# Optimization experiments

Hardware: AMD Instinct MI355X
Metric: run time of the kernel (lower is better)

The kernel has to match this reference:

```python
import jax, jax.numpy as jnp
import numpy as np

D_MODEL = 16   # output feature dim of channel_proj
D_STATE = 8
D_CONV = 2
D_INNER = 4    # expand * inner mamba d_model (2*2)
DT_RANK = 1    # ceil(2/16)
NUM_PAIRS = 36
B, W, T = 8, 8, 1024


def setup_inputs() -> dict:
    key = jax.random.key(0)
    ks = jax.random.split(key, 12)
    s = 0.5
    return {
        "raw_signals": jax.random.normal(ks[0], (B, W, NUM_PAIRS, 2, T), jnp.float32),
        "in_proj_w": jax.random.normal(ks[1], (2 * D_INNER, 2), jnp.float32) * s,
        "conv_w": jax.random.normal(ks[2], (D_INNER, D_CONV), jnp.float32) * s,
        "conv_b": jax.random.normal(ks[3], (D_INNER,), jnp.float32) * 0.1,
        "x_proj_w": jax.random.normal(ks[4], (DT_RANK + 2 * D_STATE, D_INNER), jnp.float32) * s,
        "dt_proj_w": jax.random.normal(ks[5], (D_INNER, DT_RANK), jnp.float32) * s,
        "dt_proj_b": jax.random.normal(ks[6], (D_INNER,), jnp.float32) * 0.1,
        # S4D-real init: A_log = log(arange(1..d_state)) per inner channel
        "A_log": jnp.log(jnp.broadcast_to(jnp.arange(1, D_STATE + 1, dtype=jnp.float32), (D_INNER, D_STATE))),
        "D_skip": jnp.ones((D_INNER,), jnp.float32),
        "out_proj_w": jax.random.normal(ks[7], (2, D_INNER), jnp.float32) * s,
        "proj_w": jax.random.normal(ks[8], (D_MODEL, 2), jnp.float32) * s,
        "proj_b": jax.random.normal(ks[9], (D_MODEL,), jnp.float32) * 0.1,
    }


def _mamba_forward(x_in, in_proj_w, conv_w, conv_b, x_proj_w, dt_proj_w,
                   dt_proj_b, A_log, D_skip, out_proj_w):
    # x_in: (N, T, 2)
    N, Tlen, _ = x_in.shape
    xz = jnp.einsum('ntc,dc->ntd', x_in, in_proj_w)          # (N,T,2*d_inner)
    x, z = jnp.split(xz, 2, axis=-1)                          # (N,T,d_inner) each
    # causal depthwise conv1d, kernel size D_CONV
    xp = jnp.pad(x, ((0, 0), (D_CONV - 1, 0), (0, 0)))
    x = sum(xp[:, k:k + Tlen] * conv_w[:, k] for k in range(D_CONV)) + conv_b
    x = jax.nn.silu(x)
    # input-dependent dt, B, C
    x_dbl = jnp.einsum('ntd,ed->nte', x, x_proj_w)            # (N,T,dt_rank+2*d_state)
    dt, Bm, Cm = jnp.split(x_dbl, [DT_RANK, DT_RANK + D_STATE], axis=-1)
    dt = jax.nn.softplus(jnp.einsum('ntr,dr->ntd', dt, dt_proj_w) + dt_proj_b)
    A = -jnp.exp(A_log)                                       # (d_inner,d_state)
    deltaA = jnp.exp(dt[..., None] * A)                       # (N,T,d_inner,d_state)
    deltaBx = dt[..., None] * Bm[:, :, None, :] * x[..., None]

    def step(h, inputs):
        dA_t, dBx_t, c_t = inputs
        h = dA_t * h + dBx_t                                  # (N,d_inner,d_state)
        y_t = jnp.einsum('nds,ns->nd', h, c_t)
        return h, y_t

    h0 = jnp.zeros((N, D_INNER, D_STATE), x.dtype)
    _, ys = jax.lax.scan(
        step, h0,
        (deltaA.transpose(1, 0, 2, 3), deltaBx.transpose(1, 0, 2, 3), Cm.transpose(1, 0, 2)))
    y = ys.transpose(1, 0, 2) + x * D_skip                    # (N,T,d_inner)
    y = y * jax.nn.silu(z)
    return jnp.einsum('ntd,cd->ntc', y, out_proj_w)           # (N,T,2)


def reference(raw_signals, in_proj_w, conv_w, conv_b, x_proj_w, dt_proj_w,
              dt_proj_b, A_log, D_skip, out_proj_w, proj_w, proj_b):
    Bsz, Wn, P, C, Tlen = raw_signals.shape
    # per-window loop in torch does identical math -> flatten windows into batch
    x_in = raw_signals.transpose(0, 1, 2, 4, 3).reshape(-1, Tlen, C)  # (B*W*P, T, 2)
    out = _mamba_forward(x_in, in_proj_w, conv_w, conv_b, x_proj_w, dt_proj_w,
                         dt_proj_b, A_log, D_skip, out_proj_w)
    feat = out.mean(axis=1)                                   # (B*W*P, 2)
    proj = jax.nn.relu(feat @ proj_w.T + proj_b)              # dropout is eval no-op
    proj = proj.reshape(Bsz, Wn, P, -1)                       # (B,W,P,d_model)
    return proj.mean(axis=2)                                  # (B,W,d_model)
```

## Files before the change

kernel.cpp:

```cpp
#include <hip/hip_runtime.h>


#define TT 1024
#define TC 32
#define GSEG 4
#define SEGLEN (TT / GSEG)
#define NCHUNK (SEGLEN / TC)
#define NUM_PAIRS 36
#define NSEQ 2304
#define ST 36
#define PER_HALF (TC * ST)
#define HALF_SHIFT 16
#define PER_WAVE (2 * PER_HALF + HALF_SHIFT)
#define STAGE_TOTAL (GSEG * PER_WAVE)
#define COMB_OFF STAGE_TOTAL
#define COMB_SZ (2 * GSEG * 32 * 2)
#define PART_OFF (COMB_OFF + COMB_SZ)
#define PART_SZ (2 * GSEG * 2)
#define LDS_TOTAL (PART_OFF + PART_SZ)

__device__ __forceinline__ float fast_sigmoid(float v) {
    return __builtin_amdgcn_rcpf(1.0f + __expf(-v));
}

__global__ __launch_bounds__(256, 4)
void pm_kernel(const float* __restrict__ raw,
               const float* __restrict__ in_proj_w,
               const float* __restrict__ conv_w,
               const float* __restrict__ conv_b,
               const float* __restrict__ x_proj_w,
               const float* __restrict__ dt_proj_w,
               const float* __restrict__ dt_proj_b,
               const float* __restrict__ A_log,
               const float* __restrict__ D_skip,
               const float* __restrict__ out_proj_w,
               const float* __restrict__ proj_w,
               const float* __restrict__ proj_b,
               float* __restrict__ out)
{
    __shared__ float lds[LDS_TOTAL];

    const int tid  = threadIdx.x;
    const int wid  = tid >> 6;
    const int lane = tid & 63;
    const int half = lane >> 5;
    const int lh   = lane & 31;
    const int n    = blockIdx.x * 2 + half;
    const float* rp = raw + (size_t)n * (2 * TT);

    float* stg = lds + wid * PER_WAVE + half * (PER_HALF + HALF_SHIFT);

    float ipw[8][2];
#pragma unroll
    for (int j = 0; j < 8; ++j) { ipw[j][0] = in_proj_w[2*j]; ipw[j][1] = in_proj_w[2*j+1]; }
    float cw0[4], cw1[4], cbv[4], dpw[4], dpb[4], Dsk[4], ow0[4], ow1[4];
#pragma unroll
    for (int d = 0; d < 4; ++d) {
        cw0[d] = conv_w[2*d]; cw1[d] = conv_w[2*d+1]; cbv[d] = conv_b[d];
        dpw[d] = dt_proj_w[d]; dpb[d] = dt_proj_b[d];
        Dsk[d] = D_skip[d]; ow0[d] = out_proj_w[d]; ow1[d] = out_proj_w[4+d];
    }
    float xpw[17][4];
#pragma unroll
    for (int e = 0; e < 17; ++e)
#pragma unroll
        for (int d = 0; d < 4; ++d) xpw[e][d] = x_proj_w[4*e + d];

    const float LOG2E = 1.4426950408889634f;
    const int   d_idx = lh >> 3;
    const int   s_idx = lh & 7;
    const float A2ds  = -__expf(A_log[lh]) * LOG2E;
    const float owd0  = out_proj_w[d_idx];
    const float owd1  = out_proj_w[4 + d_idx];

    float A_run = 1.0f, hB = 0.0f, W = 0.0f, S = 0.0f;
    float sacc0 = 0.f, sacc1 = 0.f;

    const int seg0 = wid * SEGLEN;

    int t0 = seg0 + lh;
    float c0  = rp[t0];
    float c1  = rp[TT + t0];
    float c0m = (t0 > 0) ? rp[t0 - 1]      : 0.0f;
    float c1m = (t0 > 0) ? rp[TT + t0 - 1] : 0.0f;

    for (int chunk = 0; chunk < NCHUNK; ++chunk) {
        float p0 = 0.f, p1 = 0.f, p0m = 0.f, p1m = 0.f;
        if (chunk + 1 < NCHUNK) {
            int tn = seg0 + (chunk + 1) * TC + lh;
            p0  = rp[tn];       p1  = rp[TT + tn];
            p0m = rp[tn - 1];   p1m = rp[TT + tn - 1];
        }

        float xz[8], xm1[4];
#pragma unroll
        for (int j = 0; j < 8; ++j) xz[j] = ipw[j][0]*c0 + ipw[j][1]*c1;
#pragma unroll
        for (int d = 0; d < 4; ++d) xm1[d] = ipw[d][0]*c0m + ipw[d][1]*c1m;

        float x[4], sz[4];
#pragma unroll
        for (int d = 0; d < 4; ++d) {
            float v = xm1[d]*cw0[d] + xz[d]*cw1[d] + cbv[d];
            x[d] = v * fast_sigmoid(v);
            float zv = xz[4 + d];
            sz[d] = zv * fast_sigmoid(zv);
        }

        float dtin = xpw[0][0]*x[0] + xpw[0][1]*x[1] + xpw[0][2]*x[2] + xpw[0][3]*x[3];
        float Bm[8], Cm[8];
#pragma unroll
        for (int s = 0; s < 8; ++s) {
            Bm[s] = xpw[1+s][0]*x[0] + xpw[1+s][1]*x[1] + xpw[1+s][2]*x[2] + xpw[1+s][3]*x[3];
            Cm[s] = xpw[9+s][0]*x[0] + xpw[9+s][1]*x[1] + xpw[9+s][2]*x[2] + xpw[9+s][3]*x[3];
        }

        float* slot = stg + lh * ST;
#pragma unroll
        for (int d = 0; d < 4; ++d) {
            float v = dtin*dpw[d] + dpb[d];
            float dt = fmaxf(v, 0.0f) + __logf(1.0f + __expf(-fabsf(v)));
            *(float4*)(slot + 4*d) = make_float4(dt, dt * x[d], sz[d], 0.0f);
            float g = x[d] * Dsk[d] * sz[d];
            sacc0 = fmaf(g, ow0[d], sacc0);
            sacc1 = fmaf(g, ow1[d], sacc1);
        }
#pragma unroll
        for (int s = 0; s < 8; ++s)
            *(float2*)(slot + 16 + 2*s) = make_float2(Bm[s], Cm[s]);

        __asm__ volatile("s_waitcnt lgkmcnt(0)" ::: "memory");

#pragma unroll
        for (int t2 = 0; t2 < TC; ++t2) {
            const float* sl = stg + t2 * ST;
            float4 dv = *(const float4*)(sl + 4*d_idx);
            float2 bc = *(const float2*)(sl + 16 + 2*s_idx);
            float a = exp2f(dv.x * A2ds);
            float b = dv.y * bc.x;
            float q = bc.y * dv.z;
            A_run *= a;
            hB = fmaf(a, hB, b);
            W  = fmaf(A_run, q, W);
            S  = fmaf(hB, q, S);
        }

        __asm__ volatile("s_waitcnt lgkmcnt(0)" ::: "memory");

        c0 = p0; c1 = p1; c0m = p0m; c1m = p1m;
    }

    float* comb = lds + COMB_OFF;
    *(float2*)(comb + ((half*GSEG + wid)*32 + lh)*2) = make_float2(A_run, hB);
    __syncthreads();

    float h_in = 0.0f;
#pragma unroll
    for (int g = 0; g < GSEG; ++g) {
        if (g < wid) {
            float2 abg = *(const float2*)(comb + ((half*GSEG + g)*32 + lh)*2);
            h_in = fmaf(abg.x, h_in, abg.y);
        }
    }

    float F = fmaf(h_in, W, S);
    float tot0 = fmaf(F, owd0, sacc0);
    float tot1 = fmaf(F, owd1, sacc1);
#pragma unroll
    for (int m = 16; m >= 1; m >>= 1) {
        tot0 += __shfl_xor(tot0, m, 64);
        tot1 += __shfl_xor(tot1, m, 64);
    }
    float* part = lds + PART_OFF;
    if (lh == 0) {
        part[(half*GSEG + wid)*2]     = tot0;
        part[(half*GSEG + wid)*2 + 1] = tot1;
    }
    __syncthreads();

    if (wid == 0 && lh < 16) {
        float f0 = 0.f, f1 = 0.f;
#pragma unroll
        for (int g = 0; g < GSEG; ++g) {
            f0 += part[(half*GSEG + g)*2];
            f1 += part[(half*GSEG + g)*2 + 1];
        }
        f0 *= (1.0f / (float)TT);
        f1 *= (1.0f / (float)TT);
        float pv = f0*proj_w[2*lh] + f1*proj_w[2*lh + 1] + proj_b[lh];
        pv = fmaxf(pv, 0.0f);
        atomicAdd(out + (n / NUM_PAIRS) * 16 + lh, pv * (1.0f / NUM_PAIRS));
    }
}

extern "C" void kernel_launch(void* const* d_in, const int* in_sizes, int n_in,
                              void* d_out, int out_size, void* d_ws, size_t ws_size,
                              hipStream_t stream)
{
    const float* raw        = (const float*)d_in[0];
    const float* in_proj_w  = (const float*)d_in[1];
    const float* conv_w     = (const float*)d_in[2];
    const float* conv_b     = (const float*)d_in[3];
    const float* x_proj_w   = (const float*)d_in[4];
    const float* dt_proj_w  = (const float*)d_in[5];
    const float* dt_proj_b  = (const float*)d_in[6];
    const float* A_log      = (const float*)d_in[7];
    const float* D_skip     = (const float*)d_in[8];
    const float* out_proj_w = (const float*)d_in[9];
    const float* proj_w     = (const float*)d_in[10];
    const float* proj_b     = (const float*)d_in[11];

    hipMemsetAsync(d_out, 0, (size_t)out_size * sizeof(float), stream);

    pm_kernel<<<dim3(NSEQ / 2), dim3(256), 0, stream>>>(
        raw, in_proj_w, conv_w, conv_b, x_proj_w, dt_proj_w, dt_proj_b,
        A_log, D_skip, out_proj_w, proj_w, proj_b, (float*)d_out);
}
```

Baseline: 145.0 us.

## Double time segments per block, pack B/C in fp16, use packed v2f FMA math

Doubles the number of time segments per sequence from 4 to 8, so each block now runs 512 threads and each wave handles a shorter segment. The B/C staging in LDS moves from fp32 to half precision, shrinking slot size. Most arithmetic is recast as two-wide vector FMAs so the compiler can emit packed fp32 instructions, and the A_run/hB/W/S recurrences are merged into vector form. The combine and partial-sum buffers reuse the staging LDS after an extra barrier. The trade-offs are fp16 rounding of B and C, a longer cross-segment combine, and higher register and LDS pressure per block.

```diff
diff --git a/kernel.cpp b/kernel.cpp
--- a/kernel.cpp
+++ b/kernel.cpp
@@ -1,29 +1,29 @@
 #include <hip/hip_runtime.h>
-
+#include <hip/hip_fp16.h>
+
+
+typedef float v2f __attribute__((ext_vector_type(2)));
 
 #define TT 1024
 #define TC 32
-#define GSEG 4
+#define GSEG 8
 #define SEGLEN (TT / GSEG)
 #define NCHUNK (SEGLEN / TC)
 #define NUM_PAIRS 36
 #define NSEQ 2304
-#define ST 36
-#define PER_HALF (TC * ST)
+
+#define SLOTF 24
+#define PER_HALF (TC * SLOTF)
 #define HALF_SHIFT 16
 #define PER_WAVE (2 * PER_HALF + HALF_SHIFT)
 #define STAGE_TOTAL (GSEG * PER_WAVE)
-#define COMB_OFF STAGE_TOTAL
-#define COMB_SZ (2 * GSEG * 32 * 2)
-#define PART_OFF (COMB_OFF + COMB_SZ)
-#define PART_SZ (2 * GSEG * 2)
-#define LDS_TOTAL (PART_OFF + PART_SZ)
-
-__device__ __forceinline__ float fast_sigmoid(float v) {
-    return __builtin_amdgcn_rcpf(1.0f + __expf(-v));
+
+__device__ __forceinline__ float fast_silu(float v) {
+    float e = __builtin_amdgcn_exp2f(v * -1.4426950408889634f);
+    return v * __builtin_amdgcn_rcpf(1.0f + e);
 }
 
-__global__ __launch_bounds__(256, 4)
+__global__ __launch_bounds__(512, 6)
 void pm_kernel(const float* __restrict__ raw,
                const float* __restrict__ in_proj_w,
                const float* __restrict__ conv_w,
@@ -38,7 +38,7 @@
                const float* __restrict__ proj_b,
                float* __restrict__ out)
 {
-    __shared__ float lds[LDS_TOTAL];
+    __shared__ float lds[STAGE_TOTAL];
 
     const int tid  = threadIdx.x;
     const int wid  = tid >> 6;
@@ -50,31 +50,44 @@
 
     float* stg = lds + wid * PER_WAVE + half * (PER_HALF + HALF_SHIFT);
 
-    float ipw[8][2];
-#pragma unroll
-    for (int j = 0; j < 8; ++j) { ipw[j][0] = in_proj_w[2*j]; ipw[j][1] = in_proj_w[2*j+1]; }
-    float cw0[4], cw1[4], cbv[4], dpw[4], dpb[4], Dsk[4], ow0[4], ow1[4];
+    v2f ipc0[4], ipc1[4];
+#pragma unroll
+    for (int k = 0; k < 4; ++k) {
+        ipc0[k] = (v2f){in_proj_w[4*k],     in_proj_w[4*k + 2]};
+        ipc1[k] = (v2f){in_proj_w[4*k + 1], in_proj_w[4*k + 3]};
+    }
+    v2f cw0p[2], cw1p[2], cbp[2];
+#pragma unroll
+    for (int k = 0; k < 2; ++k) {
+        cw0p[k] = (v2f){conv_w[4*k],     conv_w[4*k + 2]};
+        cw1p[k] = (v2f){conv_w[4*k + 1], conv_w[4*k + 3]};
+        cbp[k]  = (v2f){conv_b[2*k],     conv_b[2*k + 1]};
+    }
+    float dpw[4], dpb[4], xp0[4];
+    v2f owp[4];
+    float Dsk[4];
 #pragma unroll
     for (int d = 0; d < 4; ++d) {
-        cw0[d] = conv_w[2*d]; cw1[d] = conv_w[2*d+1]; cbv[d] = conv_b[d];
         dpw[d] = dt_proj_w[d]; dpb[d] = dt_proj_b[d];
-        Dsk[d] = D_skip[d]; ow0[d] = out_proj_w[d]; ow1[d] = out_proj_w[4+d];
-    }
-    float xpw[17][4];
-#pragma unroll
-    for (int e = 0; e < 17; ++e)
-#pragma unroll
-        for (int d = 0; d < 4; ++d) xpw[e][d] = x_proj_w[4*e + d];
+        xp0[d] = x_proj_w[d];  Dsk[d] = D_skip[d];
+        owp[d] = (v2f){out_proj_w[d], out_proj_w[4 + d]};
+    }
+    v2f xbc[8][4];
+#pragma unroll
+    for (int s = 0; s < 8; ++s)
+#pragma unroll
+        for (int d = 0; d < 4; ++d)
+            xbc[s][d] = (v2f){x_proj_w[4*(1+s) + d], x_proj_w[4*(9+s) + d]};
 
     const float LOG2E = 1.4426950408889634f;
     const int   d_idx = lh >> 3;
     const int   s_idx = lh & 7;
     const float A2ds  = -__expf(A_log[lh]) * LOG2E;
-    const float owd0  = out_proj_w[d_idx];
-    const float owd1  = out_proj_w[4 + d_idx];
-
-    float A_run = 1.0f, hB = 0.0f, W = 0.0f, S = 0.0f;
-    float sacc0 = 0.f, sacc1 = 0.f;
+    const v2f   owd   = (v2f){out_proj_w[d_idx], out_proj_w[4 + d_idx]};
+
+    v2f AhB = {1.0f, 0.0f};
+    v2f WS  = {0.0f, 0.0f};
+    v2f sacc = {0.0f, 0.0f};
 
     const int seg0 = wid * SEGLEN;
 
@@ -92,57 +105,74 @@
             p0m = rp[tn - 1];   p1m = rp[TT + tn - 1];
         }
 
-        float xz[8], xm1[4];
-#pragma unroll
-        for (int j = 0; j < 8; ++j) xz[j] = ipw[j][0]*c0 + ipw[j][1]*c1;
-#pragma unroll
-        for (int d = 0; d < 4; ++d) xm1[d] = ipw[d][0]*c0m + ipw[d][1]*c1m;
+        const v2f c0v = {c0, c0}, c1v = {c1, c1}, c0mv = {c0m, c0m}, c1mv = {c1m, c1m};
+        v2f xzp[4], xm1p[2];
+#pragma unroll
+        for (int k = 0; k < 4; ++k)
+            xzp[k] = __builtin_elementwise_fma(ipc0[k], c0v, ipc1[k] * c1v);
+#pragma unroll
+        for (int k = 0; k < 2; ++k)
+            xm1p[k] = __builtin_elementwise_fma(ipc0[k], c0mv, ipc1[k] * c1mv);
 
         float x[4], sz[4];
 #pragma unroll
+        for (int k = 0; k < 2; ++k) {
+            v2f v = __builtin_elementwise_fma(xm1p[k], cw0p[k],
+                    __builtin_elementwise_fma(xzp[k], cw1p[k], cbp[k]));
+            x[2*k]   = fast_silu(v.x);
+            x[2*k+1] = fast_silu(v.y);
+            sz[2*k]   = fast_silu(xzp[2 + k].x);
+            sz[2*k+1] = fast_silu(xzp[2 + k].y);
+        }
+
+        float dtin = xp0[0]*x[0] + xp0[1]*x[1] + xp0[2]*x[2] + xp0[3]*x[3];
+        v2f bc[8];
+#pragma unroll
+        for (int s = 0; s < 8; ++s) {
+            v2f a = xbc[s][0] * (v2f){x[0], x[0]};
+            a = __builtin_elementwise_fma(xbc[s][1], (v2f){x[1], x[1]}, a);
+            a = __builtin_elementwise_fma(xbc[s][2], (v2f){x[2], x[2]}, a);
+            bc[s] = __builtin_elementwise_fma(xbc[s][3], (v2f){x[3], x[3]}, a);
+        }
+
+        float* slot = stg + lh * SLOTF;
+#pragma unroll
         for (int d = 0; d < 4; ++d) {
-            float v = xm1[d]*cw0[d] + xz[d]*cw1[d] + cbv[d];
-            x[d] = v * fast_sigmoid(v);
-            float zv = xz[4 + d];
-            sz[d] = zv * fast_sigmoid(zv);
-        }
-
-        float dtin = xpw[0][0]*x[0] + xpw[0][1]*x[1] + xpw[0][2]*x[2] + xpw[0][3]*x[3];
-        float Bm[8], Cm[8];
-#pragma unroll
-        for (int s = 0; s < 8; ++s) {
-            Bm[s] = xpw[1+s][0]*x[0] + xpw[1+s][1]*x[1] + xpw[1+s][2]*x[2] + xpw[1+s][3]*x[3];
-            Cm[s] = xpw[9+s][0]*x[0] + xpw[9+s][1]*x[1] + xpw[9+s][2]*x[2] + xpw[9+s][3]*x[3];
-        }
-
-        float* slot = stg + lh * ST;
-#pragma unroll
-        for (int d = 0; d < 4; ++d) {
-            float v = dtin*dpw[d] + dpb[d];
-            float dt = fmaxf(v, 0.0f) + __logf(1.0f + __expf(-fabsf(v)));
+            float u = dtin*dpw[d] + dpb[d];
+            float dt = fmaxf(u, 0.0f) + __logf(1.0f + __expf(-fabsf(u)));
             *(float4*)(slot + 4*d) = make_float4(dt, dt * x[d], sz[d], 0.0f);
             float g = x[d] * Dsk[d] * sz[d];
-            sacc0 = fmaf(g, ow0[d], sacc0);
-            sacc1 = fmaf(g, ow1[d], sacc1);
-        }
-#pragma unroll
-        for (int s = 0; s < 8; ++s)
-            *(float2*)(slot + 16 + 2*s) = make_float2(Bm[s], Cm[s]);
+            sacc = __builtin_elementwise_fma((v2f){g, g}, owp[d], sacc);
+        }
+        uint4 ubc0, ubc1;
+        {
+            __half2 h0 = __floats2half2_rn(bc[0].x, bc[0].y);
+            __half2 h1 = __floats2half2_rn(bc[1].x, bc[1].y);
+            __half2 h2 = __floats2half2_rn(bc[2].x, bc[2].y);
+            __half2 h3 = __floats2half2_rn(bc[3].x, bc[3].y);
+            __half2 h4 = __floats2half2_rn(bc[4].x, bc[4].y);
+            __half2 h5 = __floats2half2_rn(bc[5].x, bc[5].y);
+            __half2 h6 = __floats2half2_rn(bc[6].x, bc[6].y);
+            __half2 h7 = __floats2half2_rn(bc[7].x, bc[7].y);
+            ubc0 = make_uint4(*(uint*)&h0, *(uint*)&h1, *(uint*)&h2, *(uint*)&h3);
+            ubc1 = make_uint4(*(uint*)&h4, *(uint*)&h5, *(uint*)&h6, *(uint*)&h7);
+        }
+        *(uint4*)(slot + 16) = ubc0;
+        *(uint4*)(slot + 20) = ubc1;
 
         __asm__ volatile("s_waitcnt lgkmcnt(0)" ::: "memory");
 
 #pragma unroll
         for (int t2 = 0; t2 < TC; ++t2) {
-            const float* sl = stg + t2 * ST;
-            float4 dv = *(const float4*)(sl + 4*d_idx);
-            float2 bc = *(const float2*)(sl + 16 + 2*s_idx);
-            float a = exp2f(dv.x * A2ds);
-            float b = dv.y * bc.x;
-            float q = bc.y * dv.z;
-            A_run *= a;
-            hB = fmaf(a, hB, b);
-            W  = fmaf(A_run, q, W);
-            S  = fmaf(hB, q, S);
+            const float* sl = stg + t2 * SLOTF;
+            float4 f = *(const float4*)(sl + 4*d_idx);
+            uint ub  = *(const uint*)(sl + 16 + s_idx);
+            float2 bcf = __half22float2(*(__half2*)&ub);
+            float a = __builtin_amdgcn_exp2f(f.x * A2ds);
+            float b = f.y * bcf.x;
+            float q = f.z * bcf.y;
+            AhB = __builtin_elementwise_fma((v2f){a, a}, AhB, (v2f){0.0f, b});
+            WS  = __builtin_elementwise_fma(AhB, (v2f){q, q}, WS);
         }
 
         __asm__ volatile("s_waitcnt lgkmcnt(0)" ::: "memory");
@@ -150,28 +180,29 @@
         c0 = p0; c1 = p1; c0m = p0m; c1m = p1m;
     }
 
-    float* comb = lds + COMB_OFF;
-    *(float2*)(comb + ((half*GSEG + wid)*32 + lh)*2) = make_float2(A_run, hB);
+    __syncthreads();
+    float2* comb = (float2*)lds;
+    comb[(half*GSEG + wid)*32 + lh] = make_float2(AhB.x, AhB.y);
     __syncthreads();
 
     float h_in = 0.0f;
 #pragma unroll
     for (int g = 0; g < GSEG; ++g) {
         if (g < wid) {
-            float2 abg = *(const float2*)(comb + ((half*GSEG + g)*32 + lh)*2);
+            float2 abg = comb[(half*GSEG + g)*32 + lh];
             h_in = fmaf(abg.x, h_in, abg.y);
         }
     }
 
-    float F = fmaf(h_in, W, S);
-    float tot0 = fmaf(F, owd0, sacc0);
-    float tot1 = fmaf(F, owd1, sacc1);
+    float F = fmaf(h_in, WS.x, WS.y);
+    v2f tot = __builtin_elementwise_fma((v2f){F, F}, owd, sacc);
+    float tot0 = tot.x, tot1 = tot.y;
 #pragma unroll
     for (int m = 16; m >= 1; m >>= 1) {
         tot0 += __shfl_xor(tot0, m, 64);
         tot1 += __shfl_xor(tot1, m, 64);
     }
-    float* part = lds + PART_OFF;
+    float* part = lds + 2048;
     if (lh == 0) {
         part[(half*GSEG + wid)*2]     = tot0;
         part[(half*GSEG + wid)*2 + 1] = tot1;
@@ -212,7 +243,7 @@
 
     hipMemsetAsync(d_out, 0, (size_t)out_size * sizeof(float), stream);
 
-    pm_kernel<<<dim3(NSEQ / 2), dim3(256), 0, stream>>>(
+    pm_kernel<<<dim3(NSEQ / 2), dim3(512), 0, stream>>>(
         raw, in_proj_w, conv_w, conv_b, x_proj_w, dt_proj_w, dt_proj_b,
         A_log, D_skip, out_proj_w, proj_w, proj_b, (float*)d_out);
 }
```

Result: faster. 133.4 us (-8.0%).

## Pack scan operands to fp16, double time segments, restructure LDS staging

Applied to the files above, without the earlier changes.

Splits each sequence into 8 time segments across 8 waves instead of 4, launching 512-thread blocks. Packs dt*x, silu(z), B and C into fp16 pairs and uses a packed half multiply in the inner scan loop. Replaces the LDS staging layout with separate dt, ds and BC arrays, the BC array padded with an odd stride. Also swaps in raw exp2/log/rcp intrinsics for silu and softplus and vectorises the B/C projection with float2 FMAs. The fp16 rounding of scan inputs lowers precision. The new softplus form can overflow for large inputs.

```diff
diff --git a/kernel.cpp b/kernel.cpp
--- a/kernel.cpp
+++ b/kernel.cpp
@@ -1,29 +1,38 @@
 #include <hip/hip_runtime.h>
-
+#include <hip/hip_fp16.h>
+
+
+typedef float v2f __attribute__((ext_vector_type(2)));
 
 #define TT 1024
 #define TC 32
-#define GSEG 4
+#define GSEG 8
 #define SEGLEN (TT / GSEG)
 #define NCHUNK (SEGLEN / TC)
 #define NUM_PAIRS 36
 #define NSEQ 2304
-#define ST 36
-#define PER_HALF (TC * ST)
-#define HALF_SHIFT 16
-#define PER_WAVE (2 * PER_HALF + HALF_SHIFT)
+
+#define DT_OFF 0
+#define DS_OFF 128
+#define BC_OFF 256
+#define BC_STRIDE 33
+#define PER_HALF_STRIDE 528
+#define PER_WAVE (2 * PER_HALF_STRIDE)
 #define STAGE_TOTAL (GSEG * PER_WAVE)
-#define COMB_OFF STAGE_TOTAL
-#define COMB_SZ (2 * GSEG * 32 * 2)
-#define PART_OFF (COMB_OFF + COMB_SZ)
-#define PART_SZ (2 * GSEG * 2)
-#define LDS_TOTAL (PART_OFF + PART_SZ)
-
-__device__ __forceinline__ float fast_sigmoid(float v) {
-    return __builtin_amdgcn_rcpf(1.0f + __expf(-v));
-}
-
-__global__ __launch_bounds__(256, 4)
+
+__device__ __forceinline__ float fast_silu(float v) {
+    float e = __builtin_amdgcn_exp2f(v * -1.4426950408889634f);
+    return v * __builtin_amdgcn_rcpf(1.0f + e);
+}
+__device__ __forceinline__ float fast_softplus(float v) {
+    float e = __builtin_amdgcn_exp2f(v * 1.4426950408889634f);
+    return __builtin_amdgcn_logf(1.0f + e) * 0.6931471805599453f;
+}
+__device__ __forceinline__ uint pk_h2(float a, float b) {
+    return __builtin_bit_cast(uint, __builtin_amdgcn_cvt_pkrtz(a, b));
+}
+
+__global__ __launch_bounds__(512, 6)
 void pm_kernel(const float* __restrict__ raw,
                const float* __restrict__ in_proj_w,
                const float* __restrict__ conv_w,
@@ -38,7 +47,7 @@
                const float* __restrict__ proj_b,
                float* __restrict__ out)
 {
-    __shared__ float lds[LDS_TOTAL];
+    __shared__ float lds[STAGE_TOTAL];
 
     const int tid  = threadIdx.x;
     const int wid  = tid >> 6;
@@ -48,23 +57,25 @@
     const int n    = blockIdx.x * 2 + half;
     const float* rp = raw + (size_t)n * (2 * TT);
 
-    float* stg = lds + wid * PER_WAVE + half * (PER_HALF + HALF_SHIFT);
-
-    float ipw[8][2];
-#pragma unroll
-    for (int j = 0; j < 8; ++j) { ipw[j][0] = in_proj_w[2*j]; ipw[j][1] = in_proj_w[2*j+1]; }
-    float cw0[4], cw1[4], cbv[4], dpw[4], dpb[4], Dsk[4], ow0[4], ow1[4];
+    float* hb = lds + wid * PER_WAVE + half * PER_HALF_STRIDE;
+
+    float ip0[8], ip1[8];
+#pragma unroll
+    for (int j = 0; j < 8; ++j) { ip0[j] = in_proj_w[2*j]; ip1[j] = in_proj_w[2*j+1]; }
+    float cw0[4], cw1[4], cbv[4], dpw[4], dpb[4], Dsk[4], ow0[4], ow1[4], xp0[4];
 #pragma unroll
     for (int d = 0; d < 4; ++d) {
         cw0[d] = conv_w[2*d]; cw1[d] = conv_w[2*d+1]; cbv[d] = conv_b[d];
         dpw[d] = dt_proj_w[d]; dpb[d] = dt_proj_b[d];
         Dsk[d] = D_skip[d]; ow0[d] = out_proj_w[d]; ow1[d] = out_proj_w[4+d];
-    }
-    float xpw[17][4];
-#pragma unroll
-    for (int e = 0; e < 17; ++e)
-#pragma unroll
-        for (int d = 0; d < 4; ++d) xpw[e][d] = x_proj_w[4*e + d];
+        xp0[d] = x_proj_w[d];
+    }
+    v2f xbc[8][4];
+#pragma unroll
+    for (int s = 0; s < 8; ++s)
+#pragma unroll
+        for (int d = 0; d < 4; ++d)
+            xbc[s][d] = (v2f){x_proj_w[4*(1+s) + d], x_proj_w[4*(9+s) + d]};
 
     const float LOG2E = 1.4426950408889634f;
     const int   d_idx = lh >> 3;
@@ -73,6 +84,10 @@
     const float owd0  = out_proj_w[d_idx];
     const float owd1  = out_proj_w[4 + d_idx];
 
+    const float* dtp = hb + DT_OFF + d_idx;
+    const uint*  dsp = (const uint*)(hb + DS_OFF) + d_idx;
+    const uint*  bcp = (const uint*)(hb + BC_OFF) + s_idx * BC_STRIDE;
+
     float A_run = 1.0f, hB = 0.0f, W = 0.0f, S = 0.0f;
     float sacc0 = 0.f, sacc1 = 0.f;
 
@@ -92,73 +107,75 @@
             p0m = rp[tn - 1];   p1m = rp[TT + tn - 1];
         }
 
-        float xz[8], xm1[4];
-#pragma unroll
-        for (int j = 0; j < 8; ++j) xz[j] = ipw[j][0]*c0 + ipw[j][1]*c1;
-#pragma unroll
-        for (int d = 0; d < 4; ++d) xm1[d] = ipw[d][0]*c0m + ipw[d][1]*c1m;
-
         float x[4], sz[4];
 #pragma unroll
         for (int d = 0; d < 4; ++d) {
-            float v = xm1[d]*cw0[d] + xz[d]*cw1[d] + cbv[d];
-            x[d] = v * fast_sigmoid(v);
-            float zv = xz[4 + d];
-            sz[d] = zv * fast_sigmoid(zv);
-        }
-
-        float dtin = xpw[0][0]*x[0] + xpw[0][1]*x[1] + xpw[0][2]*x[2] + xpw[0][3]*x[3];
-        float Bm[8], Cm[8];
+            float xz  = ip0[d]*c0  + ip1[d]*c1;
+            float xm1 = ip0[d]*c0m + ip1[d]*c1m;
+            float zv  = ip0[4+d]*c0 + ip1[4+d]*c1;
+            float v   = xm1*cw0[d] + xz*cw1[d] + cbv[d];
+            x[d]  = fast_silu(v);
+            sz[d] = fast_silu(zv);
+        }
+
+        float dtin = xp0[0]*x[0] + xp0[1]*x[1] + xp0[2]*x[2] + xp0[3]*x[3];
+
+        v2f bc[8];
 #pragma unroll
         for (int s = 0; s < 8; ++s) {
-            Bm[s] = xpw[1+s][0]*x[0] + xpw[1+s][1]*x[1] + xpw[1+s][2]*x[2] + xpw[1+s][3]*x[3];
-            Cm[s] = xpw[9+s][0]*x[0] + xpw[9+s][1]*x[1] + xpw[9+s][2]*x[2] + xpw[9+s][3]*x[3];
-        }
-
-        float* slot = stg + lh * ST;
+            v2f a = xbc[s][0] * (v2f){x[0], x[0]};
+            a = __builtin_elementwise_fma(xbc[s][1], (v2f){x[1], x[1]}, a);
+            a = __builtin_elementwise_fma(xbc[s][2], (v2f){x[2], x[2]}, a);
+            bc[s] = __builtin_elementwise_fma(xbc[s][3], (v2f){x[3], x[3]}, a);
+        }
+
+        float dt[4];
 #pragma unroll
         for (int d = 0; d < 4; ++d) {
-            float v = dtin*dpw[d] + dpb[d];
-            float dt = fmaxf(v, 0.0f) + __logf(1.0f + __expf(-fabsf(v)));
-            *(float4*)(slot + 4*d) = make_float4(dt, dt * x[d], sz[d], 0.0f);
+            dt[d] = fast_softplus(dtin*dpw[d] + dpb[d]);
             float g = x[d] * Dsk[d] * sz[d];
             sacc0 = fmaf(g, ow0[d], sacc0);
             sacc1 = fmaf(g, ow1[d], sacc1);
         }
+
+        *(float4*)(hb + DT_OFF + lh*4) = make_float4(dt[0], dt[1], dt[2], dt[3]);
+        *(uint4*)((uint*)(hb + DS_OFF) + lh*4) =
+            make_uint4(pk_h2(dt[0]*x[0], sz[0]), pk_h2(dt[1]*x[1], sz[1]),
+                       pk_h2(dt[2]*x[2], sz[2]), pk_h2(dt[3]*x[3], sz[3]));
+        uint* bcw = (uint*)(hb + BC_OFF) + lh;
 #pragma unroll
         for (int s = 0; s < 8; ++s)
-            *(float2*)(slot + 16 + 2*s) = make_float2(Bm[s], Cm[s]);
-
-        __asm__ volatile("s_waitcnt lgkmcnt(0)" ::: "memory");
+            bcw[s * BC_STRIDE] = pk_h2(bc[s].x, bc[s].y);
 
 #pragma unroll
         for (int t2 = 0; t2 < TC; ++t2) {
-            const float* sl = stg + t2 * ST;
-            float4 dv = *(const float4*)(sl + 4*d_idx);
-            float2 bc = *(const float2*)(sl + 16 + 2*s_idx);
-            float a = exp2f(dv.x * A2ds);
-            float b = dv.y * bc.x;
-            float q = bc.y * dv.z;
+            float dtv = dtp[t2*4];
+            uint  uds = dsp[t2*4];
+            uint  ubc = bcp[t2];
+            __half2 prod = __hmul2(__builtin_bit_cast(__half2, uds),
+                                   __builtin_bit_cast(__half2, ubc));
+            float b = __half2float(__low2half(prod));
+            float q = __half2float(__high2half(prod));
+            float a = __builtin_amdgcn_exp2f(dtv * A2ds);
             A_run *= a;
             hB = fmaf(a, hB, b);
             W  = fmaf(A_run, q, W);
             S  = fmaf(hB, q, S);
         }
 
-        __asm__ volatile("s_waitcnt lgkmcnt(0)" ::: "memory");
-
         c0 = p0; c1 = p1; c0m = p0m; c1m = p1m;
     }
 
-    float* comb = lds + COMB_OFF;
-    *(float2*)(comb + ((half*GSEG + wid)*32 + lh)*2) = make_float2(A_run, hB);
+    __syncthreads();
+    float2* comb = (float2*)lds;
+    comb[(half*GSEG + wid)*32 + lh] = make_float2(A_run, hB);
     __syncthreads();
 
     float h_in = 0.0f;
 #pragma unroll
     for (int g = 0; g < GSEG; ++g) {
         if (g < wid) {
-            float2 abg = *(const float2*)(comb + ((half*GSEG + g)*32 + lh)*2);
+            float2 abg = comb[(half*GSEG + g)*32 + lh];
             h_in = fmaf(abg.x, h_in, abg.y);
         }
     }
@@ -171,7 +188,7 @@
         tot0 += __shfl_xor(tot0, m, 64);
         tot1 += __shfl_xor(tot1, m, 64);
     }
-    float* part = lds + PART_OFF;
+    float* part = lds + 2048;
     if (lh == 0) {
         part[(half*GSEG + wid)*2]     = tot0;
         part[(half*GSEG + wid)*2 + 1] = tot1;
@@ -212,7 +229,7 @@
 
     hipMemsetAsync(d_out, 0, (size_t)out_size * sizeof(float), stream);
 
-    pm_kernel<<<dim3(NSEQ / 2), dim3(256), 0, stream>>>(
+    pm_kernel<<<dim3(NSEQ / 2), dim3(512), 0, stream>>>(
         raw, in_proj_w, conv_w, conv_b, x_proj_w, dt_proj_w, dt_proj_b,
         A_log, D_skip, out_proj_w, proj_w, proj_b, (float*)d_out);
 }
```

Measured after the change: 126.7 us. -12.6%, faster.
